# Kernel tuning notes

Hardware: AMD Instinct MI355X
Metric: run time of the kernel (lower is better)

The kernel has to match this reference:

```python
import jax, jax.numpy as jnp
import numpy as np

N_NODES = 100000


def graph_conv(x, src, dst, edge_weight, W_rel, b_rel, W_root):
    # PyG GraphConv: out = lin_rel(scatter_add(x[src] * w_e -> dst)) + lin_root(x)
    msg = x[src] * edge_weight[:, None]                      # [E, F] gather + scale
    agg = jax.ops.segment_sum(msg, dst, num_segments=N_NODES)  # [N, F] scatter-add
    return agg @ W_rel + b_rel + x @ W_root                  # [N, C]


def setup_inputs() -> dict:
    key = jax.random.key(0)
    k = jax.random.split(key, 8)
    F_in, H, C = 64, 64, 64
    E = 1600000
    x = jax.random.normal(k[0], (N_NODES, F_in), dtype=jnp.float32)
    edge_index = jax.random.randint(k[1], (2, E), 0, N_NODES, dtype=jnp.int64)
    edge_weight = jax.random.uniform(k[2], (E,), dtype=jnp.float32)
    s1 = 1.0 / np.sqrt(F_in)
    s2 = 1.0 / np.sqrt(H)
    W1_rel = jax.random.uniform(k[3], (F_in, H), jnp.float32, -s1, s1)
    W1_root = jax.random.uniform(k[4], (F_in, H), jnp.float32, -s1, s1)
    b1 = jnp.zeros((H,), jnp.float32)
    W2_rel = jax.random.uniform(k[5], (H, C), jnp.float32, -s2, s2)
    W2_root = jax.random.uniform(k[6], (H, C), jnp.float32, -s2, s2)
    b2 = jnp.zeros((C,), jnp.float32)
    return {"x": x, "edge_index": edge_index, "edge_weight": edge_weight,
            "W1_rel": W1_rel, "b1": b1, "W1_root": W1_root,
            "W2_rel": W2_rel, "b2": b2, "W2_root": W2_root}


def reference(x, edge_index, edge_weight, W1_rel, b1, W1_root, W2_rel, b2, W2_root):
    src, dst = edge_index[0], edge_index[1]
    h = graph_conv(x, src, dst, edge_weight, W1_rel, b1, W1_root)
    h = jax.nn.relu(h)
    out = graph_conv(h, src, dst, edge_weight, W2_rel, b2, W2_root)
    return out
```

## Files before the change

### kernel.cpp

```cpp
#include <hip/hip_runtime.h>

#define N_NODES 100000
#define F 64
#define SCAN_TPB 256
#define SCAN_ELEMS 1024

__global__ void hist_kernel(const int* __restrict__ dst, int* __restrict__ cnt, int E) {
    int i = blockIdx.x * blockDim.x + threadIdx.x;
    if (i < E) atomicAdd(&cnt[dst[i]], 1);
}

__global__ void scan1_kernel(const int* __restrict__ cnt, int* __restrict__ excl,
                             int* __restrict__ bsum, int n) {
    __shared__ int sh[SCAN_TPB];
    const int t = threadIdx.x;
    const int base = blockIdx.x * SCAN_ELEMS + t * 4;
    int v0 = (base + 0 < n) ? cnt[base + 0] : 0;
    int v1 = (base + 1 < n) ? cnt[base + 1] : 0;
    int v2 = (base + 2 < n) ? cnt[base + 2] : 0;
    int v3 = (base + 3 < n) ? cnt[base + 3] : 0;
    const int tot = v0 + v1 + v2 + v3;
    sh[t] = tot; __syncthreads();
    for (int off = 1; off < SCAN_TPB; off <<= 1) {
        int x = (t >= off) ? sh[t - off] : 0;
        __syncthreads();
        sh[t] += x;
        __syncthreads();
    }
    int exc = sh[t] - tot;
    if (t == SCAN_TPB - 1) bsum[blockIdx.x] = sh[t];
    if (base + 0 < n) excl[base + 0] = exc;  exc += v0;
    if (base + 1 < n) excl[base + 1] = exc;  exc += v1;
    if (base + 2 < n) excl[base + 2] = exc;  exc += v2;
    if (base + 3 < n) excl[base + 3] = exc;
}

__global__ void scan2_kernel(int* __restrict__ bsum, int nb) {
    __shared__ int sh[SCAN_TPB];
    const int t = threadIdx.x;
    const int v = (t < nb) ? bsum[t] : 0;
    sh[t] = v; __syncthreads();
    for (int off = 1; off < SCAN_TPB; off <<= 1) {
        int x = (t >= off) ? sh[t - off] : 0;
        __syncthreads();
        sh[t] += x;
        __syncthreads();
    }
    if (t < nb) bsum[t] = sh[t] - v;
}

__global__ void scan3_kernel(int* __restrict__ excl, const int* __restrict__ bsum,
                             int n, int E) {
    int i = blockIdx.x * blockDim.x + threadIdx.x;
    if (i < n) excl[i] += bsum[i / SCAN_ELEMS];
    if (i == 0) excl[n] = E;
}

__global__ void reorder_kernel(const int* __restrict__ src, const int* __restrict__ dst,
                               const float* __restrict__ ew, int* __restrict__ cursor,
                               int* __restrict__ eSrc, float* __restrict__ eW, int E) {
    int i = blockIdx.x * blockDim.x + threadIdx.x;
    if (i >= E) return;
    int d = dst[i];
    int pos = atomicAdd(&cursor[d], 1);
    eSrc[pos] = src[i];
    eW[pos]   = ew[i];
}

__global__ void gather_kernel(const float* __restrict__ xin, const int* __restrict__ rowptr,
                              const int* __restrict__ eSrc, const float* __restrict__ eW,
                              float* __restrict__ agg) {
    const int wid  = (blockIdx.x * blockDim.x + threadIdx.x) >> 6;
    const int lane = threadIdx.x & 63;
    if (wid >= N_NODES) return;
    int beg = __builtin_amdgcn_readfirstlane(rowptr[wid]);
    int end = __builtin_amdgcn_readfirstlane(rowptr[wid + 1]);
    float acc = 0.f;
    int e = beg;
    for (; e + 2 <= end; e += 2) {
        int   s0 = eSrc[e],   s1 = eSrc[e + 1];
        float w0 = eW[e],     w1 = eW[e + 1];
        acc += w0 * xin[(size_t)s0 * F + lane];
        acc += w1 * xin[(size_t)s1 * F + lane];
    }
    if (e < end) acc += eW[e] * xin[(size_t)eSrc[e] * F + lane];
    agg[(size_t)wid * F + lane] = acc;
}

__global__ void scatter_kernel(const float* __restrict__ xin,
                               const int* __restrict__ src,
                               const int* __restrict__ dst,
                               const float* __restrict__ ew,
                               float* __restrict__ agg, int E) {
    int gid  = blockIdx.x * blockDim.x + threadIdx.x;
    int eid  = gid >> 6;
    int lane = threadIdx.x & 63;
    if (eid >= E) return;
    float v = ew[eid] * xin[(size_t)src[eid] * F + lane];
    atomicAdd(&agg[(size_t)dst[eid] * F + lane], v);
}

template <bool RELU>
__global__ void dense_tiled(const float* __restrict__ A,
                            const float* __restrict__ X,
                            const float* __restrict__ Wrel,
                            const float* __restrict__ Wroot,
                            const float* __restrict__ bias,
                            float* __restrict__ out) {
    __shared__ float sWr[F * F];
    __shared__ float sWo[F * F];
    __shared__ float sA[F * F];
    __shared__ float sX[F * F];

    const int t = threadIdx.x;
    for (int i = t; i < 1024; i += 256) {
        reinterpret_cast<float4*>(sWr)[i] = reinterpret_cast<const float4*>(Wrel)[i];
        reinterpret_cast<float4*>(sWo)[i] = reinterpret_cast<const float4*>(Wroot)[i];
    }

    const int row0 = blockIdx.x * 64;
    for (int i = t; i < 1024; i += 256) {
        const int r  = i >> 4;
        const int c4 = (i & 15) << 2;
        int rr = row0 + r; if (rr > N_NODES - 1) rr = N_NODES - 1;
        const float4 av = *reinterpret_cast<const float4*>(A + (size_t)rr * F + c4);
        const float4 xv = *reinterpret_cast<const float4*>(X + (size_t)rr * F + c4);
        const int rbase = r * F, rx = r & 31;
        sA[rbase + ((c4 + 0) ^ rx)] = av.x;
        sA[rbase + ((c4 + 1) ^ rx)] = av.y;
        sA[rbase + ((c4 + 2) ^ rx)] = av.z;
        sA[rbase + ((c4 + 3) ^ rx)] = av.w;
        sX[rbase + ((c4 + 0) ^ rx)] = xv.x;
        sX[rbase + ((c4 + 1) ^ rx)] = xv.y;
        sX[rbase + ((c4 + 2) ^ rx)] = xv.z;
        sX[rbase + ((c4 + 3) ^ rx)] = xv.w;
    }
    __syncthreads();

    const int cg = (t & 15) << 2;
    const int rg = (t >> 4) << 2;
    float acc[4][4];
    {
        const float b0 = bias[cg], b1 = bias[cg + 1], b2 = bias[cg + 2], b3 = bias[cg + 3];
#pragma unroll
        for (int i = 0; i < 4; ++i) { acc[i][0] = b0; acc[i][1] = b1; acc[i][2] = b2; acc[i][3] = b3; }
    }
    int rbase[4], rxs[4];
#pragma unroll
    for (int i = 0; i < 4; ++i) { rbase[i] = (rg + i) * F; rxs[i] = (rg + i) & 31; }

#pragma unroll 4
    for (int k = 0; k < F; ++k) {
        const float4 wr = *reinterpret_cast<const float4*>(&sWr[k * F + cg]);
        const float4 wo = *reinterpret_cast<const float4*>(&sWo[k * F + cg]);
#pragma unroll
        for (int i = 0; i < 4; ++i) {
            const float a  = sA[rbase[i] + (k ^ rxs[i])];
            const float xv = sX[rbase[i] + (k ^ rxs[i])];
            acc[i][0] += a * wr.x + xv * wo.x;
            acc[i][1] += a * wr.y + xv * wo.y;
            acc[i][2] += a * wr.z + xv * wo.z;
            acc[i][3] += a * wr.w + xv * wo.w;
        }
    }

#pragma unroll
    for (int i = 0; i < 4; ++i) {
        const int n = row0 + rg + i;
        if (n < N_NODES) {
            float4 o;
            o.x = acc[i][0]; o.y = acc[i][1]; o.z = acc[i][2]; o.w = acc[i][3];
            if (RELU) {
                o.x = fmaxf(o.x, 0.f); o.y = fmaxf(o.y, 0.f);
                o.z = fmaxf(o.z, 0.f); o.w = fmaxf(o.w, 0.f);
            }
            *reinterpret_cast<float4*>(out + (size_t)n * F + cg) = o;
        }
    }
}

extern "C" void kernel_launch(void* const* d_in, const int* in_sizes, int n_in,
                              void* d_out, int out_size, void* d_ws, size_t ws_size,
                              hipStream_t stream) {
    const float* x   = (const float*)d_in[0];
    const int*   ei  = (const int*)d_in[1];
    const float* ew  = (const float*)d_in[2];
    const float* W1r = (const float*)d_in[3];
    const float* b1  = (const float*)d_in[4];
    const float* W1o = (const float*)d_in[5];
    const float* W2r = (const float*)d_in[6];
    const float* b2  = (const float*)d_in[7];
    const float* W2o = (const float*)d_in[8];
    float*       out = (float*)d_out;

    const int E = in_sizes[2];
    const int* src = ei;
    const int* dst = ei + E;

    const int nScanBlocks = (N_NODES + SCAN_ELEMS - 1) / SCAN_ELEMS;
    const size_t aggB = (size_t)N_NODES * F * sizeof(float);
    const size_t eB   = (size_t)E * 4;
    const size_t rpB  = (((size_t)(N_NODES + 1) * 4) + 15) & ~(size_t)15;
    const size_t curB = (((size_t)N_NODES * 4) + 15) & ~(size_t)15;
    const size_t bsB  = (((size_t)nScanBlocks * 4) + 15) & ~(size_t)15;

    char* p = (char*)d_ws;
    float* agg    = (float*)p;  p += aggB;
    int*   eSrc   = (int*)p;    p += eB;
    float* eWgt   = (float*)p;  p += eB;
    int*   rowptr = (int*)p;    p += rpB;
    int*   cursor = (int*)p;    p += curB;
    int*   bsum   = (int*)p;    p += bsB;
    const size_t need = (size_t)(p - (char*)d_ws);

    const int denseBlocks  = (N_NODES + 63) / 64;
    const int gatherBlocks = (N_NODES * 64) / 256;

    if (ws_size >= need) {
        hipMemsetAsync(cursor, 0, (size_t)N_NODES * 4, stream);
        hist_kernel<<<(E + 255) / 256, 256, 0, stream>>>(dst, cursor, E);
        scan1_kernel<<<nScanBlocks, SCAN_TPB, 0, stream>>>(cursor, rowptr, bsum, N_NODES);
        scan2_kernel<<<1, SCAN_TPB, 0, stream>>>(bsum, nScanBlocks);
        scan3_kernel<<<(N_NODES + 255) / 256, 256, 0, stream>>>(rowptr, bsum, N_NODES, E);
        hipMemcpyAsync(cursor, rowptr, (size_t)N_NODES * 4, hipMemcpyDeviceToDevice, stream);
        reorder_kernel<<<(E + 255) / 256, 256, 0, stream>>>(src, dst, ew, cursor, eSrc, eWgt, E);

        gather_kernel<<<gatherBlocks, 256, 0, stream>>>(x, rowptr, eSrc, eWgt, agg);
        dense_tiled<true><<<denseBlocks, 256, 0, stream>>>(agg, x, W1r, W1o, b1, out);

        gather_kernel<<<gatherBlocks, 256, 0, stream>>>(out, rowptr, eSrc, eWgt, agg);
        dense_tiled<false><<<denseBlocks, 256, 0, stream>>>(agg, out, W2r, W2o, b2, out);
    } else {
        const int scatterBlocks = (int)(((long long)E * 64 + 255) / 256);
        hipMemsetAsync(agg, 0, aggB, stream);
        scatter_kernel<<<scatterBlocks, 256, 0, stream>>>(x, src, dst, ew, agg, E);
        dense_tiled<true><<<denseBlocks, 256, 0, stream>>>(agg, x, W1r, W1o, b1, out);
        hipMemsetAsync(agg, 0, aggB, stream);
        scatter_kernel<<<scatterBlocks, 256, 0, stream>>>(out, src, dst, ew, agg, E);
        dense_tiled<false><<<denseBlocks, 256, 0, stream>>>(agg, out, W2r, W2o, b2, out);
    }
}
```

Before: 536.6 us.

## Reorder edges via permutation indices and widen gather accumulation to eight edges

The CSR build now scatters only an edge-index permutation instead of scattering src and weight separately. When workspace allows, src and weight are packed into int2 pairs that the gather reads indirectly through the permutation. The gather loop is unrolled to eight independent edges with separate accumulators to raise memory-level parallelism, and the cursor copy is fused into scan3. The indirect, random pair reads replace the contiguous eSrc/eW reads the gather had before, which may cost more than the cheaper reorder saves.

```diff
diff --git a/kernel.cpp b/kernel.cpp
--- a/kernel.cpp
+++ b/kernel.cpp
@@ -50,54 +50,70 @@
 }
 
 __global__ void scan3_kernel(int* __restrict__ excl, const int* __restrict__ bsum,
-                             int n, int E) {
-    int i = blockIdx.x * blockDim.x + threadIdx.x;
-    if (i < n) excl[i] += bsum[i / SCAN_ELEMS];
+                             int* __restrict__ cursor, int n, int E) {
+    int i = blockIdx.x * blockDim.x + threadIdx.x;
+    if (i < n) {
+        int v = excl[i] + bsum[i / SCAN_ELEMS];
+        excl[i]  = v;
+        cursor[i] = v;
+    }
     if (i == 0) excl[n] = E;
 }
 
-__global__ void reorder_kernel(const int* __restrict__ src, const int* __restrict__ dst,
-                               const float* __restrict__ ew, int* __restrict__ cursor,
-                               int* __restrict__ eSrc, float* __restrict__ eW, int E) {
+__global__ void pack_kernel(const int* __restrict__ src, const float* __restrict__ ew,
+                            int2* __restrict__ pair, int E) {
+    int i = blockIdx.x * blockDim.x + threadIdx.x;
+    if (i < E) pair[i] = make_int2(src[i], __float_as_int(ew[i]));
+}
+
+__global__ void reorder_perm(const int* __restrict__ dst, int* __restrict__ cursor,
+                             int* __restrict__ perm, int E) {
     int i = blockIdx.x * blockDim.x + threadIdx.x;
     if (i >= E) return;
-    int d = dst[i];
-    int pos = atomicAdd(&cursor[d], 1);
-    eSrc[pos] = src[i];
-    eW[pos]   = ew[i];
-}
-
+    int pos = atomicAdd(&cursor[dst[i]], 1);
+    perm[pos] = i;
+}
+
+template <bool PACKED>
 __global__ void gather_kernel(const float* __restrict__ xin, const int* __restrict__ rowptr,
-                              const int* __restrict__ eSrc, const float* __restrict__ eW,
+                              const int* __restrict__ perm, const int2* __restrict__ pair,
+                              const int* __restrict__ srcA, const float* __restrict__ ewA,
                               float* __restrict__ agg) {
     const int wid  = (blockIdx.x * blockDim.x + threadIdx.x) >> 6;
     const int lane = threadIdx.x & 63;
     if (wid >= N_NODES) return;
-    int beg = __builtin_amdgcn_readfirstlane(rowptr[wid]);
-    int end = __builtin_amdgcn_readfirstlane(rowptr[wid + 1]);
-    float acc = 0.f;
+    const int beg = __builtin_amdgcn_readfirstlane(rowptr[wid]);
+    const int end = __builtin_amdgcn_readfirstlane(rowptr[wid + 1]);
+    float a[8] = {0.f, 0.f, 0.f, 0.f, 0.f, 0.f, 0.f, 0.f};
     int e = beg;
-    for (; e + 2 <= end; e += 2) {
-        int   s0 = eSrc[e],   s1 = eSrc[e + 1];
-        float w0 = eW[e],     w1 = eW[e + 1];
-        acc += w0 * xin[(size_t)s0 * F + lane];
-        acc += w1 * xin[(size_t)s1 * F + lane];
-    }
-    if (e < end) acc += eW[e] * xin[(size_t)eSrc[e] * F + lane];
-    agg[(size_t)wid * F + lane] = acc;
-}
-
-__global__ void scatter_kernel(const float* __restrict__ xin,
-                               const int* __restrict__ src,
-                               const int* __restrict__ dst,
-                               const float* __restrict__ ew,
-                               float* __restrict__ agg, int E) {
-    int gid  = blockIdx.x * blockDim.x + threadIdx.x;
-    int eid  = gid >> 6;
-    int lane = threadIdx.x & 63;
-    if (eid >= E) return;
-    float v = ew[eid] * xin[(size_t)src[eid] * F + lane];
-    atomicAdd(&agg[(size_t)dst[eid] * F + lane], v);
+    for (; e + 8 <= end; e += 8) {
+        int   s[8];
+        float w[8];
+#pragma unroll
+        for (int j = 0; j < 8; ++j) {
+            const int i = perm[e + j];
+            if (PACKED) {
+                const int2 p = pair[i];
+                s[j] = p.x; w[j] = __int_as_float(p.y);
+            } else {
+                s[j] = srcA[i]; w[j] = ewA[i];
+            }
+        }
+#pragma unroll
+        for (int j = 0; j < 8; ++j)
+            a[j] += w[j] * xin[(size_t)s[j] * F + lane];
+    }
+    for (; e < end; ++e) {
+        const int i = perm[e];
+        if (PACKED) {
+            const int2 p = pair[i];
+            a[0] += __int_as_float(p.y) * xin[(size_t)p.x * F + lane];
+        } else {
+            a[0] += ewA[i] * xin[(size_t)srcA[i] * F + lane];
+        }
+    }
+    agg[(size_t)wid * F + lane] =
+        ((a[0] + a[1]) + (a[2] + a[3])) + ((a[4] + a[5]) + (a[6] + a[7]));
 }
 
 template <bool RELU>
@@ -179,6 +195,19 @@
     }
 }
 
+__global__ void scatter_kernel(const float* __restrict__ xin,
+                               const int* __restrict__ src,
+                               const int* __restrict__ dst,
+                               const float* __restrict__ ew,
+                               float* __restrict__ agg, int E) {
+    int gid  = blockIdx.x * blockDim.x + threadIdx.x;
+    int eid  = gid >> 6;
+    int lane = threadIdx.x & 63;
+    if (eid >= E) return;
+    float v = ew[eid] * xin[(size_t)src[eid] * F + lane];
+    atomicAdd(&agg[(size_t)dst[eid] * F + lane], v);
+}
+
 extern "C" void kernel_launch(void* const* d_in, const int* in_sizes, int n_in,
                               void* d_out, int out_size, void* d_ws, size_t ws_size,
                               hipStream_t stream) {
@@ -198,38 +227,49 @@
     const int* dst = ei + E;
 
     const int nScanBlocks = (N_NODES + SCAN_ELEMS - 1) / SCAN_ELEMS;
-    const size_t aggB = (size_t)N_NODES * F * sizeof(float);
-    const size_t eB   = (size_t)E * 4;
-    const size_t rpB  = (((size_t)(N_NODES + 1) * 4) + 15) & ~(size_t)15;
-    const size_t curB = (((size_t)N_NODES * 4) + 15) & ~(size_t)15;
-    const size_t bsB  = (((size_t)nScanBlocks * 4) + 15) & ~(size_t)15;
+    const size_t aggB  = (size_t)N_NODES * F * sizeof(float);
+    const size_t permB = (size_t)E * 4;
+    const size_t pairB = (size_t)E * 8;
+    const size_t rpB   = (((size_t)(N_NODES + 1) * 4) + 15) & ~(size_t)15;
+    const size_t curB  = (((size_t)N_NODES * 4) + 15) & ~(size_t)15;
+    const size_t bsB   = (((size_t)nScanBlocks * 4) + 15) & ~(size_t)15;
 
     char* p = (char*)d_ws;
     float* agg    = (float*)p;  p += aggB;
-    int*   eSrc   = (int*)p;    p += eB;
-    float* eWgt   = (float*)p;  p += eB;
+    int*   perm   = (int*)p;    p += permB;
     int*   rowptr = (int*)p;    p += rpB;
     int*   cursor = (int*)p;    p += curB;
     int*   bsum   = (int*)p;    p += bsB;
-    const size_t need = (size_t)(p - (char*)d_ws);
-
-    const int denseBlocks  = (N_NODES + 63) / 64;
-    const int gatherBlocks = (N_NODES * 64) / 256;
-
-    if (ws_size >= need) {
+    const size_t needBase = (size_t)(p - (char*)d_ws);
+    int2*  pair   = (int2*)p;
+    const size_t needPair = needBase + pairB;
+
+    const int denseBlocks   = (N_NODES + 63) / 64;
+    const int gatherBlocks  = (N_NODES * 64) / 256;
+    const int edgeBlocks    = (E + 255) / 256;
+
+    if (ws_size >= needBase) {
+        const bool packed = (ws_size >= needPair);
         hipMemsetAsync(cursor, 0, (size_t)N_NODES * 4, stream);
-        hist_kernel<<<(E + 255) / 256, 256, 0, stream>>>(dst, cursor, E);
+        hist_kernel<<<edgeBlocks, 256, 0, stream>>>(dst, cursor, E);
         scan1_kernel<<<nScanBlocks, SCAN_TPB, 0, stream>>>(cursor, rowptr, bsum, N_NODES);
         scan2_kernel<<<1, SCAN_TPB, 0, stream>>>(bsum, nScanBlocks);
-        scan3_kernel<<<(N_NODES + 255) / 256, 256, 0, stream>>>(rowptr, bsum, N_NODES, E);
-        hipMemcpyAsync(cursor, rowptr, (size_t)N_NODES * 4, hipMemcpyDeviceToDevice, stream);
-        reorder_kernel<<<(E + 255) / 256, 256, 0, stream>>>(src, dst, ew, cursor, eSrc, eWgt, E);
-
-        gather_kernel<<<gatherBlocks, 256, 0, stream>>>(x, rowptr, eSrc, eWgt, agg);
-        dense_tiled<true><<<denseBlocks, 256, 0, stream>>>(agg, x, W1r, W1o, b1, out);
-
-        gather_kernel<<<gatherBlocks, 256, 0, stream>>>(out, rowptr, eSrc, eWgt, agg);
-        dense_tiled<false><<<denseBlocks, 256, 0, stream>>>(agg, out, W2r, W2o, b2, out);
+        scan3_kernel<<<(N_NODES + 255) / 256, 256, 0, stream>>>(rowptr, bsum, cursor, N_NODES, E);
+        if (packed)
+            pack_kernel<<<edgeBlocks, 256, 0, stream>>>(src, ew, pair, E);
+        reorder_perm<<<edgeBlocks, 256, 0, stream>>>(dst, cursor, perm, E);
+
+        if (packed) {
+            gather_kernel<true><<<gatherBlocks, 256, 0, stream>>>(x, rowptr, perm, pair, src, ew, agg);
+            dense_tiled<true><<<denseBlocks, 256, 0, stream>>>(agg, x, W1r, W1o, b1, out);
+            gather_kernel<true><<<gatherBlocks, 256, 0, stream>>>(out, rowptr, perm, pair, src, ew, agg);
+            dense_tiled<false><<<denseBlocks, 256, 0, stream>>>(agg, out, W2r, W2o, b2, out);
+        } else {
+            gather_kernel<false><<<gatherBlocks, 256, 0, stream>>>(x, rowptr, perm, nullptr, src, ew, agg);
+            dense_tiled<true><<<denseBlocks, 256, 0, stream>>>(agg, x, W1r, W1o, b1, out);
+            gather_kernel<false><<<gatherBlocks, 256, 0, stream>>>(out, rowptr, perm, nullptr, src, ew, agg);
+            dense_tiled<false><<<denseBlocks, 256, 0, stream>>>(agg, out, W2r, W2o, b2, out);
+        }
     } else {
         const int scatterBlocks = (int)(((long long)E * 64 + 255) / 256);
         hipMemsetAsync(agg, 0, aggB, stream);
```

After: 597.7 us. 11.4% more time.
